# Kernel optimization log

Measured on AMD Instinct MI355X. Metric: run time of the kernel, lower is better.

The kernel has to match this reference:

```python
import jax, jax.numpy as jnp
import numpy as np

N = 100000      # nodes
E = 3200000     # edges per sparse operator (avg degree 32)
IN = 256        # in_features
OUT = 64        # out_features


def spmm(idx, val, x):
    # COO sparse-dense matmul: out[r] += val * x[c]
    return jax.ops.segment_sum(val[:, None] * x[idx[1]], idx[0], num_segments=x.shape[0])


def setup_inputs() -> dict:
    key = jax.random.key(0)
    ks = jax.random.split(key, 12)
    return {
        "x": jax.random.normal(ks[0], (N, IN), jnp.float32),
        "W": jax.random.normal(ks[1], (IN, OUT), jnp.float32) * 0.05,
        "a": jax.random.normal(ks[2], (6, 2 * OUT), jnp.float32) * 0.05,
        "A_idx": jax.random.randint(ks[3], (2, E), 0, N),
        "A_val": jax.random.uniform(ks[4], (E,), jnp.float32) * (1.0 / 32.0),
        "P1_idx": jax.random.randint(ks[5], (2, E), 0, N),
        "P1_val": jax.random.normal(ks[6], (E,), jnp.float32) * (1.0 / 32.0),
        "P2_idx": jax.random.randint(ks[7], (2, E), 0, N),
        "P2_val": jax.random.normal(ks[8], (E,), jnp.float32) * (1.0 / 32.0),
        "P3_idx": jax.random.randint(ks[9], (2, E), 0, N),
        "P3_val": jax.random.normal(ks[10], (E,), jnp.float32) * (1.0 / 32.0),
    }


def reference(x, W, a, A_idx, A_val, P1_idx, P1_val, P2_idx, P2_val, P3_idx, P3_val):
    s0 = x @ W                                   # [N, OUT]
    n, f = s0.shape
    h_A = spmm(A_idx, A_val, s0)
    h_A2 = spmm(A_idx, A_val, h_A)
    h_A3 = spmm(A_idx, A_val, h_A2)
    h_s1 = jnp.abs(spmm(P1_idx, P1_val, s0))
    h_s2 = jnp.abs(spmm(P2_idx, P2_val, s0))
    h_s3 = jnp.abs(spmm(P3_idx, P3_val, s0))
    chans = [h_A, h_A2, h_A3, h_s1, h_s2, h_s3]
    # Faithful to torch: cat([h, h_x], dim=0).view(N, 2F) is a raw memory
    # reflatten of the stacked (2N, F) buffer, NOT a per-node feature concat.
    e = jnp.stack(
        [jnp.concatenate([s0, hx], axis=0).reshape(n, 2 * f) @ a[i]
         for i, hx in enumerate(chans)], axis=1)  # [N, 6]
    attention = jax.nn.softmax(e, axis=1)         # [N, 6]
    # Faithful to torch: cat(dim=2) -> (N, F, 6), then .view(N, 6, F) is a
    # raw reshape (memory reinterpretation), not a transpose.
    h_all = jnp.stack(chans, axis=2).reshape(n, 6, f)   # [N, 6, F]
    h_prime = jnp.mean(attention[:, :, None] * h_all, axis=1)  # [N, F]
    return h_prime, attention
```

## Files before the change

kernel.cpp:

```cpp
#include <hip/hip_runtime.h>
#include <math.h>

#define IN_F 256
#define OUT_F 64
#define RPB 256
#define NBKT_MAX 512
#define BIN_C 8192
#define BIN_T 512

typedef unsigned int uint2v __attribute__((ext_vector_type(2)));

__global__ __launch_bounds__(256) void zero_i_kernel(int* __restrict__ p, int n) {
  int t = blockIdx.x * blockDim.x + threadIdx.x;
  int stride = gridDim.x * blockDim.x;
  for (; t < n; t += stride) p[t] = 0;
}

__global__ __launch_bounds__(256) void gemm_kernel(const float* __restrict__ x,
    const float* __restrict__ W, float* __restrict__ s0, int N) {
  __shared__ float4 Wt4[64 * 64];
  float* Wtf = (float*)Wt4;
  for (int idx = threadIdx.x; idx < 64 * 256; idx += 256) {
    int k = idx >> 6, n = idx & 63;
    Wtf[(n * 64 + ((k >> 2) ^ n)) * 4 + (k & 3)] = W[idx];
  }
  __syncthreads();
  int lane = threadIdx.x & 63;
  int gw = (blockIdx.x * 256 + threadIdx.x) >> 6;
  int nw = (gridDim.x * 256) >> 6;
  const float4* wrow = &Wt4[lane * 64];
  for (int r = gw; r < N; r += nw) {
    int ru = __builtin_amdgcn_readfirstlane(r);
    const float4* xr = (const float4*)(x + (size_t)ru * IN_F);
    float acc = 0.f;
#pragma unroll 8
    for (int k4 = 0; k4 < 64; ++k4) {
      float4 xv = xr[k4];
      float4 wv = wrow[k4 ^ lane];
      acc = fmaf(xv.x, wv.x, acc);
      acc = fmaf(xv.y, wv.y, acc);
      acc = fmaf(xv.z, wv.z, acc);
      acc = fmaf(xv.w, wv.w, acc);
    }
    s0[(size_t)ru * OUT_F + lane] = acc;
  }
}

__global__ __launch_bounds__(BIN_T) void bin_kernel(
    const int* __restrict__ r0, const int* __restrict__ r1,
    const int* __restrict__ r2, const int* __restrict__ r3,
    const float* __restrict__ v0, const float* __restrict__ v1,
    const float* __restrict__ v2, const float* __restrict__ v3,
    int* __restrict__ bcur, uint2* __restrict__ PB, int E, int nbkt, int cap,
    int op_off) {
  int op = blockIdx.y + op_off;
  const int* rows = (op == 0) ? r0 : (op == 1) ? r1 : (op == 2) ? r2 : r3;
  const float* val = (op == 0) ? v0 : (op == 1) ? v1 : (op == 2) ? v2 : v3;
  const int* cols = rows + E;
  uint2* So = PB + (size_t)blockIdx.y * nbkt * cap;
  int* cur = bcur + blockIdx.y * nbkt;

  __shared__ uint2 st[BIN_C];
  __shared__ int h[NBKT_MAX];
  __shared__ int lbase[NBKT_MAX + 1];
  __shared__ int lcur[NBKT_MAX];
  __shared__ int sc[BIN_T];

  int base = blockIdx.x * BIN_C;
  int cnt = min(BIN_C, E - base);

  for (int i = threadIdx.x; i < nbkt; i += BIN_T) h[i] = 0;
  __syncthreads();
  for (int i = threadIdx.x; i < cnt; i += BIN_T)
    atomicAdd(&h[rows[base + i] >> 8], 1);
  __syncthreads();
  int v = (threadIdx.x < nbkt) ? h[threadIdx.x] : 0;
  sc[threadIdx.x] = v;
  __syncthreads();
  for (int s = 1; s < BIN_T; s <<= 1) {
    int u = (threadIdx.x >= s) ? sc[threadIdx.x - s] : 0;
    __syncthreads();
    sc[threadIdx.x] += u;
    __syncthreads();
  }
  if (threadIdx.x < nbkt) {
    int ex = sc[threadIdx.x] - v;
    lbase[threadIdx.x] = ex;
    lcur[threadIdx.x] = ex;
  }
  if (threadIdx.x == 0) lbase[nbkt] = cnt;
  __syncthreads();
  for (int i = threadIdx.x; i < cnt; i += BIN_T) {
    int r = rows[base + i];
    int bk = r >> 8;
    unsigned p = (unsigned)cols[base + i] | ((unsigned)(r & 255) << 17);
    int slot = atomicAdd(&lcur[bk], 1);
    st[slot] = make_uint2(p, __float_as_uint(val[base + i]));
  }
  __syncthreads();
  for (int bk = threadIdx.x; bk < nbkt; bk += BIN_T) {
    int c = lbase[bk + 1] - lbase[bk];
    int pos = 0;
    if (c) {
      pos = atomicAdd(&cur[bk], c);
      if (pos + c > cap) pos = (cap > c) ? (cap - c) : 0;
    }
    h[bk] = bk * cap + pos;
  }
  __syncthreads();
  for (int j = threadIdx.x; j < cnt; j += BIN_T) {
    int lo = 0, hi = nbkt;
    while (hi - lo > 1) {
      int mid = (lo + hi) >> 1;
      if (lbase[mid] <= j) lo = mid; else hi = mid;
    }
    So[(size_t)h[lo] + (j - lbase[lo])] = st[j];
  }
}

__global__ __launch_bounds__(512) void bscan_kernel(const int* __restrict__ bcnt,
    int* __restrict__ bbase, int nbkt) {
  int op = blockIdx.x;
  const int* c = bcnt + op * nbkt;
  int* bb = bbase + op * (nbkt + 1);
  __shared__ int sb[512];
  int t = threadIdx.x;
  int v = (t < nbkt) ? c[t] : 0;
  sb[t] = v;
  __syncthreads();
  for (int s = 1; s < 512; s <<= 1) {
    int u = (t >= s) ? sb[t - s] : 0;
    __syncthreads();
    sb[t] += u;
    __syncthreads();
  }
  if (t < nbkt) bb[t] = sb[t] - v;
  if (t == 0) bb[nbkt] = sb[nbkt - 1];
}

__global__ __launch_bounds__(512) void bucket_sort_kernel(
    const uint2* __restrict__ PB, const int* __restrict__ bcnt,
    const int* __restrict__ bbase, uint2* __restrict__ dst,
    int* __restrict__ off, int E, int N, int nbkt, int cap) {
  PB    += (size_t)blockIdx.y * nbkt * cap;
  bcnt  += blockIdx.y * nbkt;
  bbase += blockIdx.y * (nbkt + 1);
  dst   += (size_t)blockIdx.y * E;
  off   += (size_t)blockIdx.y * N;
  int b = blockIdx.x;
  const uint2* src = PB + (size_t)b * cap;
  int cnt = min(bcnt[b], cap);
  int s = bbase[b];
  int rowbase = b << 8;
  int nrows = min(RPB, N - rowbase);

  __shared__ int rcnt[RPB];
  __shared__ int rend[RPB];
  __shared__ int lcur[RPB];
  if (threadIdx.x < RPB) rcnt[threadIdx.x] = 0;
  __syncthreads();
  for (int i = threadIdx.x; i < cnt; i += 512)
    atomicAdd(&rcnt[src[i].x >> 17], 1);
  __syncthreads();
  if (threadIdx.x < RPB) rend[threadIdx.x] = rcnt[threadIdx.x];
  __syncthreads();
  for (int st = 1; st < RPB; st <<= 1) {
    int u = 0;
    if (threadIdx.x < RPB && threadIdx.x >= st) u = rend[threadIdx.x - st];
    __syncthreads();
    if (threadIdx.x < RPB) rend[threadIdx.x] += u;
    __syncthreads();
  }
  if (threadIdx.x < nrows) off[rowbase + threadIdx.x] = s + rend[threadIdx.x];
  if (threadIdx.x < RPB)
    lcur[threadIdx.x] = s + rend[threadIdx.x] - rcnt[threadIdx.x];
  __syncthreads();
  for (int i = threadIdx.x; i < cnt; i += 512) {
    uint2 rec = src[i];
    int pos = atomicAdd(&lcur[rec.x >> 17], 1);
    dst[pos] = make_uint2(rec.x & 0x1FFFFu, rec.y);
  }
}

__global__ __launch_bounds__(256) void spmm_gather(const uint2* __restrict__ S,
    const int* __restrict__ offEnd, const float* __restrict__ xin,
    float* __restrict__ out, int N, int Estride, int remap) {
  int op = blockIdx.y;
  S      += (size_t)op * Estride;
  offEnd += (size_t)op * N;
  int ch = remap ? ((op == 0) ? 0 : (op + 2)) : op;
  out    += (size_t)ch * (size_t)N * OUT_F;
  int lane = threadIdx.x & 63;
  int r = (blockIdx.x * 256 + threadIdx.x) >> 6;
  if (r >= N) return;
  r = __builtin_amdgcn_readfirstlane(r);
  int s = (r == 0) ? 0 : offEnd[r - 1];
  int e = offEnd[r];
  float acc = 0.f;
  for (int base = s; base < e; base += 64) {
    int m = e - base;
    if (m > 64) m = 64;
    uint2v rec = (uint2v)0u;
    if (lane < m)
      rec = __builtin_nontemporal_load((const uint2v*)S + (base + lane));
    int k = 0;
    for (; k + 8 <= m; k += 8) {
#pragma unroll
      for (int u = 0; u < 8; ++u) {
        int c = __shfl((int)rec.x, k + u);
        float w = __uint_as_float((unsigned)__shfl((int)rec.y, k + u));
        acc = fmaf(w, xin[(size_t)(unsigned)c * OUT_F + lane], acc);
      }
    }
    for (; k < m; ++k) {
      int c = __shfl((int)rec.x, k);
      float w = __uint_as_float((unsigned)__shfl((int)rec.y, k));
      acc = fmaf(w, xin[(size_t)(unsigned)c * OUT_F + lane], acc);
    }
  }
  __builtin_nontemporal_store(acc, &out[(size_t)r * OUT_F + lane]);
}

__global__ __launch_bounds__(256) void fuse_kernel(const float* __restrict__ s0,
    const float* __restrict__ chan, const float* __restrict__ a,
    float* __restrict__ out_h, float* __restrict__ out_att, int N) {
  int lane = threadIdx.x & 63;
  int i = (blockIdx.x * blockDim.x + threadIdx.x) >> 6;
  if (i >= N) return;
  size_t NF = (size_t)N * OUT_F;
  float e[6];
  int half = N >> 1;
  if (i < half) {
    float lo = s0[(size_t)(2 * i) * OUT_F + lane];
    float hi = s0[(size_t)(2 * i + 1) * OUT_F + lane];
#pragma unroll
    for (int ch = 0; ch < 6; ++ch) {
      float p = fmaf(lo, a[ch * 128 + lane], hi * a[ch * 128 + 64 + lane]);
#pragma unroll
      for (int off = 32; off; off >>= 1) p += __shfl_xor(p, off);
      e[ch] = p;
    }
  } else {
    int r = 2 * i - N;
#pragma unroll
    for (int ch = 0; ch < 6; ++ch) {
      float lo = chan[(size_t)ch * NF + (size_t)r * OUT_F + lane];
      float hi = chan[(size_t)ch * NF + (size_t)(r + 1) * OUT_F + lane];
      if (ch >= 3) { lo = fabsf(lo); hi = fabsf(hi); }
      float p = fmaf(lo, a[ch * 128 + lane], hi * a[ch * 128 + 64 + lane]);
#pragma unroll
      for (int off = 32; off; off >>= 1) p += __shfl_xor(p, off);
      e[ch] = p;
    }
  }
  float m = e[0];
#pragma unroll
  for (int ch = 1; ch < 6; ++ch) m = fmaxf(m, e[ch]);
  float s = 0.f;
#pragma unroll
  for (int ch = 0; ch < 6; ++ch) { e[ch] = expf(e[ch] - m); s += e[ch]; }
  float inv = 1.f / s;
#pragma unroll
  for (int ch = 0; ch < 6; ++ch) e[ch] *= inv;

  if (lane < 6) {
    float v = e[0];
    if (lane == 1) v = e[1];
    if (lane == 2) v = e[2];
    if (lane == 3) v = e[3];
    if (lane == 4) v = e[4];
    if (lane == 5) v = e[5];
    out_att[(size_t)i * 6 + lane] = v;
  }

  float hp = 0.f;
#pragma unroll
  for (int p = 0; p < 6; ++p) {
    int idx = p * 64 + lane;
    int c = idx % 6;
    int j = idx / 6;
    float v = chan[(size_t)c * NF + (size_t)i * OUT_F + j];
    v = (c >= 3) ? fabsf(v) : v;
    hp = fmaf(e[p], v, hp);
  }
  out_h[(size_t)i * OUT_F + lane] = hp * (1.f / 6.f);
}

extern "C" void kernel_launch(void* const* d_in, const int* in_sizes, int n_in,
                              void* d_out, int out_size, void* d_ws, size_t ws_size,
                              hipStream_t stream) {
  const float* x      = (const float*)d_in[0];
  const float* W      = (const float*)d_in[1];
  const float* a      = (const float*)d_in[2];
  const int*   A_idx  = (const int*)d_in[3];
  const float* A_val  = (const float*)d_in[4];
  const int*   P1_idx = (const int*)d_in[5];
  const float* P1_val = (const float*)d_in[6];
  const int*   P2_idx = (const int*)d_in[7];
  const float* P2_val = (const float*)d_in[8];
  const int*   P3_idx = (const int*)d_in[9];
  const float* P3_val = (const float*)d_in[10];

  int N = in_sizes[0] / IN_F;
  int E = in_sizes[4];
  int nbkt = (N + RPB - 1) / RPB;

  size_t NF = (size_t)N * OUT_F;
  float* s0   = (float*)d_ws;
  float* chan = s0 + NF;
  float* hA   = chan + 0 * NF;
  float* hA2  = chan + 1 * NF;
  float* hA3  = chan + 2 * NF;
  float* hs1  = chan + 3 * NF;

  float* out_h   = (float*)d_out;
  float* out_att = out_h + NF;

  int fblocks = (N * 64 + 255) / 256;
  int gblocks = (N * 64 + 255) / 256;
  int binblocks = (E + BIN_C - 1) / BIN_C;

  int cap = E / nbkt + E / (4 * nbkt) + 256;
  size_t pbcap_max = (6 * NF * 4) / ((size_t)4 * nbkt * 8);
  if ((size_t)cap > pbcap_max) cap = (int)pbcap_max;

  gemm_kernel<<<512, 256, 0, stream>>>(x, W, s0, N);

  uint2* PB   = (uint2*)chan;
  uint2* S    = (uint2*)(chan + 6 * NF);
  int* off    = (int*)(S + (size_t)4 * E);
  int* bcur   = off + 4 * N;
  int* bbase  = bcur + 4 * nbkt;
  size_t need = (size_t)((char*)(bbase + 4 * (nbkt + 1)) - (char*)d_ws);

  if (ws_size >= need) {
    zero_i_kernel<<<4, 256, 0, stream>>>(bcur, 4 * nbkt);
    bin_kernel<<<dim3(binblocks, 4), BIN_T, 0, stream>>>(A_idx, P1_idx, P2_idx,
        P3_idx, A_val, P1_val, P2_val, P3_val, bcur, PB, E, nbkt, cap, 0);
    bscan_kernel<<<4, 512, 0, stream>>>(bcur, bbase, nbkt);
    bucket_sort_kernel<<<dim3(nbkt, 4), 512, 0, stream>>>(PB, bcur, bbase, S,
        off, E, N, nbkt, cap);
    spmm_gather<<<dim3(gblocks, 4), 256, 0, stream>>>(S, off, s0, chan, N, E, 1);
    spmm_gather<<<dim3(gblocks, 1), 256, 0, stream>>>(S, off, hA,  hA2, N, 0, 0);
    spmm_gather<<<dim3(gblocks, 1), 256, 0, stream>>>(S, off, hA2, hA3, N, 0, 0);
  } else {
    uint2* S1    = (uint2*)(chan + 6 * NF);
    uint2* PB1   = S1 + E;
    int* off1    = (int*)(PB1 + (size_t)nbkt * cap);
    int* bcur1   = off1 + 4 * N;
    int* bbase1  = bcur1 + nbkt;
    for (int o = 0; o < 4; ++o) {
      zero_i_kernel<<<1, 256, 0, stream>>>(bcur1, nbkt);
      bin_kernel<<<dim3(binblocks, 1), BIN_T, 0, stream>>>(A_idx, P1_idx, P2_idx,
          P3_idx, A_val, P1_val, P2_val, P3_val, bcur1, PB1, E, nbkt, cap, o);
      bscan_kernel<<<1, 512, 0, stream>>>(bcur1, bbase1, nbkt);
      bucket_sort_kernel<<<dim3(nbkt, 1), 512, 0, stream>>>(PB1, bcur1, bbase1,
          S1, off1 + o * N, E, N, nbkt, cap);
      if (o == 0) {
        spmm_gather<<<dim3(gblocks, 1), 256, 0, stream>>>(S1, off1, s0,  hA,  N, 0, 0);
        spmm_gather<<<dim3(gblocks, 1), 256, 0, stream>>>(S1, off1, hA,  hA2, N, 0, 0);
        spmm_gather<<<dim3(gblocks, 1), 256, 0, stream>>>(S1, off1, hA2, hA3, N, 0, 0);
      } else {
        spmm_gather<<<dim3(gblocks, 1), 256, 0, stream>>>(S1, off1 + o * N, s0,
            hs1 + (size_t)(o - 1) * NF, N, 0, 0);
      }
    }
  }

  fuse_kernel<<<fblocks, 256, 0, stream>>>(s0, chan, a, out_h, out_att, N);
}
```

Baseline: 1.535 ms.

## Register-block the x@W GEMM over four rows per wave with LDS-staged inputs

Each wave now handles four rows per iteration instead of one. The four x rows are loaded with one coalesced float4 per lane into a per-wave LDS buffer, and each W float4 read from LDS feeds four accumulators. This is meant to cut the per-row scalar or broadcast global loads and reuse each W LDS read across four rows. There is no barrier between the LDS stores and the reads within the wave, so correctness relies on wave-synchronous execution. Rows past the end of N leave stale LDS data in use, but those results are never stored.

```diff
diff --git a/kernel.cpp b/kernel.cpp
--- a/kernel.cpp
+++ b/kernel.cpp
@@ -19,6 +19,7 @@
 __global__ __launch_bounds__(256) void gemm_kernel(const float* __restrict__ x,
     const float* __restrict__ W, float* __restrict__ s0, int N) {
   __shared__ float4 Wt4[64 * 64];
+  __shared__ float4 xb[4][4][64];
   float* Wtf = (float*)Wt4;
   for (int idx = threadIdx.x; idx < 64 * 256; idx += 256) {
     int k = idx >> 6, n = idx & 63;
@@ -26,23 +27,45 @@
   }
   __syncthreads();
   int lane = threadIdx.x & 63;
+  int wv = threadIdx.x >> 6;
   int gw = (blockIdx.x * 256 + threadIdx.x) >> 6;
   int nw = (gridDim.x * 256) >> 6;
   const float4* wrow = &Wt4[lane * 64];
-  for (int r = gw; r < N; r += nw) {
-    int ru = __builtin_amdgcn_readfirstlane(r);
-    const float4* xr = (const float4*)(x + (size_t)ru * IN_F);
-    float acc = 0.f;
+  float4 (*myx)[64] = xb[wv];
+
+  for (int g = gw; g * 4 < N; g += nw) {
+    int r0 = g * 4;
+    int nr = N - r0; if (nr > 4) nr = 4;
+    float4 rw0, rw1, rw2, rw3;
+    rw0 = ((const float4*)(x + (size_t)r0 * IN_F))[lane];
+    if (nr > 1) rw1 = ((const float4*)(x + (size_t)(r0 + 1) * IN_F))[lane];
+    if (nr > 2) rw2 = ((const float4*)(x + (size_t)(r0 + 2) * IN_F))[lane];
+    if (nr > 3) rw3 = ((const float4*)(x + (size_t)(r0 + 3) * IN_F))[lane];
+    myx[0][lane] = rw0;
+    if (nr > 1) myx[1][lane] = rw1;
+    if (nr > 2) myx[2][lane] = rw2;
+    if (nr > 3) myx[3][lane] = rw3;
+    float a0 = 0.f, a1 = 0.f, a2 = 0.f, a3 = 0.f;
 #pragma unroll 8
     for (int k4 = 0; k4 < 64; ++k4) {
-      float4 xv = xr[k4];
-      float4 wv = wrow[k4 ^ lane];
-      acc = fmaf(xv.x, wv.x, acc);
-      acc = fmaf(xv.y, wv.y, acc);
-      acc = fmaf(xv.z, wv.z, acc);
-      acc = fmaf(xv.w, wv.w, acc);
-    }
-    s0[(size_t)ru * OUT_F + lane] = acc;
+      float4 w4 = wrow[k4 ^ lane];
+      float4 xv = myx[0][k4];
+      a0 = fmaf(xv.x, w4.x, a0); a0 = fmaf(xv.y, w4.y, a0);
+      a0 = fmaf(xv.z, w4.z, a0); a0 = fmaf(xv.w, w4.w, a0);
+      xv = myx[1][k4];
+      a1 = fmaf(xv.x, w4.x, a1); a1 = fmaf(xv.y, w4.y, a1);
+      a1 = fmaf(xv.z, w4.z, a1); a1 = fmaf(xv.w, w4.w, a1);
+      xv = myx[2][k4];
+      a2 = fmaf(xv.x, w4.x, a2); a2 = fmaf(xv.y, w4.y, a2);
+      a2 = fmaf(xv.z, w4.z, a2); a2 = fmaf(xv.w, w4.w, a2);
+      xv = myx[3][k4];
+      a3 = fmaf(xv.x, w4.x, a3); a3 = fmaf(xv.y, w4.y, a3);
+      a3 = fmaf(xv.z, w4.z, a3); a3 = fmaf(xv.w, w4.w, a3);
+    }
+    s0[(size_t)r0 * OUT_F + lane] = a0;
+    if (nr > 1) s0[(size_t)(r0 + 1) * OUT_F + lane] = a1;
+    if (nr > 2) s0[(size_t)(r0 + 2) * OUT_F + lane] = a2;
+    if (nr > 3) s0[(size_t)(r0 + 3) * OUT_F + lane] = a3;
   }
 }
 
```

After: 1.266 ms. 17.5% less time.
